# Kernel optimization log

Measured on AMD Instinct MI355X. Metric: run time of the kernel, lower is better.

Reference implementation:

```python
import jax, jax.numpy as jnp
import numpy as np

B, T, E, H, S = 64, 128, 256, 512, 1024


def setup_inputs() -> dict:
    key = jax.random.key(0)
    ks = jax.random.split(key, 14)
    p = lambda k, shape, s=0.05: jax.random.normal(k, shape, dtype=jnp.float32) * s
    return {
        "embedded_inputs": jax.random.normal(ks[0], (B, T, E), dtype=jnp.float32),
        "h0": jax.random.normal(ks[1], (B, H), dtype=jnp.float32),
        "c0": jax.random.normal(ks[2], (B, H), dtype=jnp.float32),
        "context": jax.random.normal(ks[3], (B, S, H), dtype=jnp.float32),
        "W_ih": p(ks[4], (E, 4 * H)),
        "b_ih": p(ks[5], (4 * H,)),
        "W_hh": p(ks[6], (H, 4 * H)),
        "b_hh": p(ks[7], (4 * H,)),
        "W_out": p(ks[8], (2 * H, H)),
        "b_out": p(ks[9], (H,)),
        "W_ax": p(ks[10], (H + E, H)),
        "b_ax": p(ks[11], (H,)),
        "W_pg": p(ks[12], (4 * H, 1)),
        "b_pg": p(ks[13], (1,)),
    }


def reference(embedded_inputs, h0, c0, context, W_ih, b_ih, W_hh, b_hh,
              W_out, b_out, W_ax, b_ax, W_pg, b_pg):
    # mask positions where the encoder output is all-zero padding
    ctx_mask = jnp.mean(context, axis=-1) == 0  # [B,S]

    def step(carry, x):  # x: [B,E]
        h, c = carry
        gates = x @ W_ih + b_ih + h @ W_hh + b_hh          # [B,4H]
        i, f, g, o = jnp.split(gates, 4, axis=-1)
        c_t = jax.nn.sigmoid(f) * c + jax.nn.sigmoid(i) * jnp.tanh(g)
        h_t = jax.nn.sigmoid(o) * jnp.tanh(c_t)            # [B,H]
        # dot attention
        scores = jnp.einsum('bsh,bh->bs', context, h_t)    # [B,S]
        scores = jnp.where(ctx_mask, -jnp.inf, scores)
        attn_dist = jax.nn.softmax(scores, axis=1)         # [B,S]
        attn_ctx = jnp.einsum('bsh,bs->bh', context, attn_dist)  # [B,H]
        xa = jnp.concatenate([attn_ctx, x], axis=-1) @ W_ax + b_ax   # [B,H]
        out = jnp.concatenate([attn_ctx, h_t], axis=-1) @ W_out + b_out  # [B,H]
        p_gen = jax.nn.sigmoid(
            jnp.concatenate([attn_ctx, h_t, c_t, xa], axis=-1) @ W_pg + b_pg)  # [B,1]
        return (h_t, c_t), (out, attn_dist, p_gen)

    xs = jnp.swapaxes(embedded_inputs, 0, 1)  # [T,B,E]
    (h, c), (outputs, attn_dists, p_gens) = jax.lax.scan(step, (h0, c0), xs)
    return outputs, h, c, attn_dists, p_gens
```

## Files before the change

kernel.cpp:

```cpp
#include <hip/hip_runtime.h>

#define T_ 128
#define B_ 64
#define E_ 256
#define H_ 512
#define S_ 1024
#define G_ 2048
#define NCH 6
#define NBLK 512
#define ABLK 128
#define BLK 256
#define NGRP 16
#define BH (B_*H_)
#define PSTR 520
#define PARTBUF (B_*NCH*PSTR)

#define U_ARR   256
#define U_TOTAL (U_ARR + NBLK*16)

#define F_V1   8704
#define F_VX   (F_V1 + 512)
#define F_S0   (F_VX + 256)
#define F_H3   (F_S0 + 64)
#define F_C3   (F_H3 + 3*BH)
#define F_SC2  (F_C3 + 3*BH)
#define F_PART (F_SC2 + 2*B_*S_)
#define F_CTX16 (F_PART + 2*PARTBUF)
#define WS_MIN_BYTES ((size_t)F_CTX16*4)
#define WS_BF16_BYTES ((size_t)F_CTX16*4 + (size_t)B_*S_*H_*2)

#define O_OUT 0
#define O_H   ((size_t)T_*B_*H_)
#define O_C   (O_H + BH)
#define O_AD  (O_C + BH)
#define O_PG  (O_AD + (size_t)T_*B_*S_)

#define S_ACT   0
#define S_PART  3088
#define S_GATE  4112
#define SB_RED  0
#define SB_ML   2080
#define SB_BIAS 2088
#define C_ACTX  5136
#define C_H2    5648
#define C_PRT   6160
#define C_TMP   6416
#define C_V1    6424
#define POOLSZ  7200

#define NEG_INF (-__builtin_inff())

__device__ __forceinline__ float sigm(float x){ return 1.f/(1.f+__expf(-x)); }
__device__ __forceinline__ float tanh_(float x){ return 1.f - 2.f/(1.f+__expf(2.f*x)); }
__device__ __forceinline__ float wred(float v){
#pragma unroll
  for (int m = 1; m < 64; m <<= 1) v += __shfl_xor(v, m, 64);
  return v;
}
__device__ __forceinline__ float ald(const float* p){
  return __hip_atomic_load(p, __ATOMIC_RELAXED, __HIP_MEMORY_SCOPE_AGENT);
}
__device__ __forceinline__ void ast(float* p, float v){
  __hip_atomic_store(p, v, __ATOMIC_RELAXED, __HIP_MEMORY_SCOPE_AGENT);
}
__device__ __forceinline__ void ast64(unsigned long long* p, unsigned long long v){
  __hip_atomic_store(p, v, __ATOMIC_RELAXED, __HIP_MEMORY_SCOPE_AGENT);
}
__device__ __forceinline__ unsigned short b16rne(float f){
  unsigned u = __float_as_uint(f);
  unsigned r = u + 0x7fffu + ((u >> 16) & 1u);
  return (unsigned short)(r >> 16);
}
__device__ __forceinline__ void unp(unsigned w, float& lo, float& hi){
  lo = __uint_as_float(w << 16);
  hi = __uint_as_float(w & 0xffff0000u);
}

__device__ __forceinline__ void gbar(unsigned* W, unsigned ep){
  __syncthreads();
  const int tid = threadIdx.x, bid = blockIdx.x;
  if (tid == 0) {
    asm volatile("s_waitcnt vmcnt(0)" ::: "memory");
    __hip_atomic_store(&W[U_ARR + bid*16], ep, __ATOMIC_RELAXED, __HIP_MEMORY_SCOPE_AGENT);
  }
  if (bid == 0) {
    const int i0 = tid*2, i1 = i0+1;
    while (__hip_atomic_load(&W[U_ARR + i0*16], __ATOMIC_RELAXED, __HIP_MEMORY_SCOPE_AGENT) < ep)
      __builtin_amdgcn_s_sleep(2);
    while (__hip_atomic_load(&W[U_ARR + i1*16], __ATOMIC_RELAXED, __HIP_MEMORY_SCOPE_AGENT) < ep)
      __builtin_amdgcn_s_sleep(2);
    __syncthreads();
    if (tid < NGRP)
      __hip_atomic_store(&W[tid*16], ep, __ATOMIC_RELAXED, __HIP_MEMORY_SCOPE_AGENT);
  }
  if (tid == 0) {
    while (__hip_atomic_load(&W[(bid>>5)*16], __ATOMIC_RELAXED, __HIP_MEMORY_SCOPE_AGENT) < ep)
      __builtin_amdgcn_s_sleep(4);
  }
  __syncthreads();
}

__device__ void do_A(int t, int bid, int tid,
                     const float* __restrict__ emb, const float* __restrict__ Wih,
                     const float* __restrict__ bih, const float* __restrict__ Whh,
                     const float* __restrict__ bhh, float* __restrict__ F,
                     float* __restrict__ pool)
{
  const int bg = bid >> 3, ug = bid & 7;
  {
    const int r = tid >> 6, i = tid & 63;
    const float* xr = emb + ((size_t)(bg*4 + r)*T_ + t)*E_ + i*4;
    *(float4*)(pool + S_ACT + r*772 + i*4) = *(const float4*)xr;
    const float* hsrc = F + F_H3 + ((t+2)%3)*BH + (size_t)(bg*4 + r)*H_ + i*8;
    float4 h0v, h1v;
    h0v.x=ald(hsrc+0); h0v.y=ald(hsrc+1); h0v.z=ald(hsrc+2); h0v.w=ald(hsrc+3);
    h1v.x=ald(hsrc+4); h1v.y=ald(hsrc+5); h1v.z=ald(hsrc+6); h1v.w=ald(hsrc+7);
    *(float4*)(pool + S_ACT + r*772 + 256 + i*8)     = h0v;
    *(float4*)(pool + S_ACT + r*772 + 256 + i*8 + 4) = h1v;
  }
  __syncthreads();
  const int ks = tid >> 7, bl = (tid >> 5) & 3, cq = tid & 31;
  const int cgi1 = cq, cgi2 = cq + 32;
  const int col1 = ((cgi1 >> 4) << 9) + ug*64 + ((cgi1 & 15) << 2);
  const int col2 = ((cgi2 >> 4) << 9) + ug*64 + ((cgi2 & 15) << 2);
  float4 A1, A2;
  if (ks == 0) {
    const float4 x1 = *(const float4*)(bih + col1), y1 = *(const float4*)(bhh + col1);
    const float4 x2 = *(const float4*)(bih + col2), y2 = *(const float4*)(bhh + col2);
    A1.x=x1.x+y1.x; A1.y=x1.y+y1.y; A1.z=x1.z+y1.z; A1.w=x1.w+y1.w;
    A2.x=x2.x+y2.x; A2.y=x2.y+y2.y; A2.z=x2.z+y2.z; A2.w=x2.w+y2.w;
  } else { A1.x=A1.y=A1.z=A1.w=0.f; A2.x=A2.y=A2.z=A2.w=0.f; }
  const float* ap = pool + S_ACT + bl*772;
  if (ks == 0) {
    const float* w1 = Wih + col1; const float* w2 = Wih + col2;
#pragma unroll 8
    for (int k = 0; k < 256; ++k) {
      float a = ap[k];
      float4 v1 = *(const float4*)(w1 + (size_t)k*G_);
      float4 v2 = *(const float4*)(w2 + (size_t)k*G_);
      A1.x=fmaf(a,v1.x,A1.x); A1.y=fmaf(a,v1.y,A1.y); A1.z=fmaf(a,v1.z,A1.z); A1.w=fmaf(a,v1.w,A1.w);
      A2.x=fmaf(a,v2.x,A2.x); A2.y=fmaf(a,v2.y,A2.y); A2.z=fmaf(a,v2.z,A2.z); A2.w=fmaf(a,v2.w,A2.w);
    }
    const float* u1 = Whh + col1; const float* u2 = Whh + col2;
    const float* ap2 = ap + 256;
#pragma unroll 8
    for (int k = 0; k < 128; ++k) {
      float a = ap2[k];
      float4 v1 = *(const float4*)(u1 + (size_t)k*G_);
      float4 v2 = *(const float4*)(u2 + (size_t)k*G_);
      A1.x=fmaf(a,v1.x,A1.x); A1.y=fmaf(a,v1.y,A1.y); A1.z=fmaf(a,v1.z,A1.z); A1.w=fmaf(a,v1.w,A1.w);
      A2.x=fmaf(a,v2.x,A2.x); A2.y=fmaf(a,v2.y,A2.y); A2.z=fmaf(a,v2.z,A2.z); A2.w=fmaf(a,v2.w,A2.w);
    }
  } else {
    const float* u1 = Whh + (size_t)128*G_ + col1; const float* u2 = Whh + (size_t)128*G_ + col2;
    const float* ap2 = ap + 384;
#pragma unroll 8
    for (int k = 0; k < 384; ++k) {
      float a = ap2[k];
      float4 v1 = *(const float4*)(u1 + (size_t)k*G_);
      float4 v2 = *(const float4*)(u2 + (size_t)k*G_);
      A1.x=fmaf(a,v1.x,A1.x); A1.y=fmaf(a,v1.y,A1.y); A1.z=fmaf(a,v1.z,A1.z); A1.w=fmaf(a,v1.w,A1.w);
      A2.x=fmaf(a,v2.x,A2.x); A2.y=fmaf(a,v2.y,A2.y); A2.z=fmaf(a,v2.z,A2.z); A2.w=fmaf(a,v2.w,A2.w);
    }
  }
  if (ks == 1) {
    *(float4*)(pool + S_PART + ((bl*64 + cgi1) << 2)) = A1;
    *(float4*)(pool + S_PART + ((bl*64 + cgi2) << 2)) = A2;
  }
  __syncthreads();
  if (ks == 0) {
    const float4 P1 = *(const float4*)(pool + S_PART + ((bl*64 + cgi1) << 2));
    const float4 P2 = *(const float4*)(pool + S_PART + ((bl*64 + cgi2) << 2));
    A1.x+=P1.x; A1.y+=P1.y; A1.z+=P1.z; A1.w+=P1.w;
    A2.x+=P2.x; A2.y+=P2.y; A2.z+=P2.z; A2.w+=P2.w;
    *(float4*)(pool + S_GATE + bl*256 + (cgi1 << 2)) = A1;
    *(float4*)(pool + S_GATE + bl*256 + (cgi2 << 2)) = A2;
  }
  __syncthreads();
  {
    const int bl2 = tid >> 6, ul = tid & 63;
    const int b2 = bg*4 + bl2, uu = ug*64 + ul;
    float gi = pool[S_GATE + bl2*256 + ul];
    float gf = pool[S_GATE + bl2*256 + 64 + ul];
    float gg = pool[S_GATE + bl2*256 + 128 + ul];
    float go = pool[S_GATE + bl2*256 + 192 + ul];
    float cp = ald(F + F_C3 + ((t+2)%3)*BH + (size_t)b2*H_ + uu);
    float cn = sigm(gf)*cp + sigm(gi)*tanh_(gg);
    float hn = sigm(go)*tanh_(cn);
    ast(F + F_H3 + (t%3)*BH + (size_t)b2*H_ + uu, hn);
    ast(F + F_C3 + (t%3)*BH + (size_t)b2*H_ + uu, cn);
  }
}

template<bool BF16>
__device__ void do_B(int t, int bid, int tid, const float* __restrict__ ctx,
                     float* __restrict__ F, float* __restrict__ pool)
{
  const int idx = bid - ABLK;
  const int b = idx / NCH, ch = idx - b*NCH;
  const int sb = (ch*S_)/NCH, se = ((ch+1)*S_)/NCH;
  const int w = tid >> 6, lane = tid & 63;
  const float* hb = F + F_H3 + (t%3)*BH + (size_t)b*H_ + lane*8;
  float h0_=ald(hb+0), h1_=ald(hb+1), h2_=ald(hb+2), h3_=ald(hb+3),
        h4_=ald(hb+4), h5_=ald(hb+5), h6_=ald(hb+6), h7_=ald(hb+7);
  float* scw = F + F_SC2 + (size_t)(t&1)*(B_*S_) + (size_t)b*S_;
  const float* s_bias = pool + SB_BIAS;

  if (BF16) {
    const uint4* c16v = (const uint4*)(F + F_CTX16) + (size_t)b*S_*64 + lane;
    float l = 0.f;
    float a0=0,a1=0,a2=0,a3=0,a4=0,a5=0,a6=0,a7=0;
    for (int s0 = sb + w*8; s0 < se; s0 += 32) {
      uint4 q[8];
#pragma unroll
      for (int i = 0; i < 8; ++i) {
        int s = s0 + i;
        int ss = (s < se) ? s : sb;
        q[i] = c16v[(size_t)ss*64];
      }
      float d[8];
#pragma unroll
      for (int i = 0; i < 8; ++i) {
        float c0,c1,c2,c3,c4,c5,c6,c7;
        unp(q[i].x,c0,c1); unp(q[i].y,c2,c3); unp(q[i].z,c4,c5); unp(q[i].w,c6,c7);
        d[i] = c0*h0_+c1*h1_+c2*h2_+c3*h3_+c4*h4_+c5*h5_+c6*h6_+c7*h7_;
      }
#pragma unroll
      for (int mm = 1; mm < 64; mm <<= 1) {
        d[0]+=__shfl_xor(d[0],mm,64); d[1]+=__shfl_xor(d[1],mm,64);
        d[2]+=__shfl_xor(d[2],mm,64); d[3]+=__shfl_xor(d[3],mm,64);
        d[4]+=__shfl_xor(d[4],mm,64); d[5]+=__shfl_xor(d[5],mm,64);
        d[6]+=__shfl_xor(d[6],mm,64); d[7]+=__shfl_xor(d[7],mm,64);
      }
      float wg[8];
#pragma unroll
      for (int i = 0; i < 8; ++i) {
        int s = s0 + i;
        bool v = (s < se);
        float bias = v ? s_bias[s - sb] : NEG_INF;
        float sc = d[i] + bias;
        if (lane == 0 && v) ast(scw + s, sc);
        wg[i] = (bias == 0.f) ? __expf(fminf(sc, 80.f)) : 0.f;
        l += wg[i];
      }
#pragma unroll
      for (int i = 0; i < 8; ++i) {
        float c0,c1,c2,c3,c4,c5,c6,c7;
        unp(q[i].x,c0,c1); unp(q[i].y,c2,c3); unp(q[i].z,c4,c5); unp(q[i].w,c6,c7);
        a0=fmaf(wg[i],c0,a0); a1=fmaf(wg[i],c1,a1); a2=fmaf(wg[i],c2,a2); a3=fmaf(wg[i],c3,a3);
        a4=fmaf(wg[i],c4,a4); a5=fmaf(wg[i],c5,a5); a6=fmaf(wg[i],c6,a6); a7=fmaf(wg[i],c7,a7);
      }
    }
    if (lane == 0) pool[SB_ML + w] = l;
    { float* r = pool + SB_RED + w*520 + lane*8;
      r[0]=a0; r[1]=a1; r[2]=a2; r[3]=a3; r[4]=a4; r[5]=a5; r[6]=a6; r[7]=a7; }
    __syncthreads();
    float lb = pool[SB_ML+0]+pool[SB_ML+1]+pool[SB_ML+2]+pool[SB_ML+3];
    float* Pp = F + F_PART + (size_t)(t&1)*PARTBUF + (size_t)(b*NCH+ch)*PSTR;
    for (int u = tid; u < H_; u += BLK)
      ast(Pp + 8 + u, pool[SB_RED + 0*520 + u] + pool[SB_RED + 1*520 + u]
                    + pool[SB_RED + 2*520 + u] + pool[SB_RED + 3*520 + u]);
    if (tid == 0) { ast(Pp+0, 0.f); ast(Pp+1, lb); }
    return;
  }

  const float* cbase = ctx + (size_t)b*S_*H_ + lane*8;
  float m = NEG_INF, l = 0.f;
  float a0=0,a1=0,a2=0,a3=0,a4=0,a5=0,a6=0,a7=0;
  for (int s0 = sb + w*4; s0 < se; s0 += 16) {
    float cv[4][8]; float d[4];
#pragma unroll
    for (int i = 0; i < 4; ++i) {
      int s = s0 + i;
      const float* cr = cbase + (size_t)(s < se ? s : sb)*H_;
      float4 cA = *(const float4*)cr, cB = *(const float4*)(cr + 4);
      cv[i][0]=cA.x; cv[i][1]=cA.y; cv[i][2]=cA.z; cv[i][3]=cA.w;
      cv[i][4]=cB.x; cv[i][5]=cB.y; cv[i][6]=cB.z; cv[i][7]=cB.w;
    }
#pragma unroll
    for (int i = 0; i < 4; ++i)
      d[i] = cv[i][0]*h0_ + cv[i][1]*h1_ + cv[i][2]*h2_ + cv[i][3]*h3_
           + cv[i][4]*h4_ + cv[i][5]*h5_ + cv[i][6]*h6_ + cv[i][7]*h7_;
#pragma unroll
    for (int mm = 1; mm < 64; mm <<= 1) {
      d[0] += __shfl_xor(d[0], mm, 64); d[1] += __shfl_xor(d[1], mm, 64);
      d[2] += __shfl_xor(d[2], mm, 64); d[3] += __shfl_xor(d[3], mm, 64);
    }
    float sc[4];
#pragma unroll
    for (int i = 0; i < 4; ++i) {
      int s = s0 + i;
      sc[i] = (s < se) ? d[i] + s_bias[s - sb] : NEG_INF;
      if (lane == 0 && s < se) ast(scw + s, sc[i]);
    }
    float mx = fmaxf(fmaxf(sc[0],sc[1]), fmaxf(sc[2],sc[3]));
    float mn = fmaxf(m, mx);
    float al = (mn == m) ? 1.f : __expf(m - mn);
    float w0 = (sc[0]==NEG_INF)?0.f:__expf(sc[0]-mn);
    float w1 = (sc[1]==NEG_INF)?0.f:__expf(sc[1]-mn);
    float w2 = (sc[2]==NEG_INF)?0.f:__expf(sc[2]-mn);
    float w3 = (sc[3]==NEG_INF)?0.f:__expf(sc[3]-mn);
    l = l*al + (w0+w1+w2+w3);
    a0 = a0*al + w0*cv[0][0] + w1*cv[1][0] + w2*cv[2][0] + w3*cv[3][0];
    a1 = a1*al + w0*cv[0][1] + w1*cv[1][1] + w2*cv[2][1] + w3*cv[3][1];
    a2 = a2*al + w0*cv[0][2] + w1*cv[1][2] + w2*cv[2][2] + w3*cv[3][2];
    a3 = a3*al + w0*cv[0][3] + w1*cv[1][3] + w2*cv[2][3] + w3*cv[3][3];
    a4 = a4*al + w0*cv[0][4] + w1*cv[1][4] + w2*cv[2][4] + w3*cv[3][4];
    a5 = a5*al + w0*cv[0][5] + w1*cv[1][5] + w2*cv[2][5] + w3*cv[3][5];
    a6 = a6*al + w0*cv[0][6] + w1*cv[1][6] + w2*cv[2][6] + w3*cv[3][6];
    a7 = a7*al + w0*cv[0][7] + w1*cv[1][7] + w2*cv[2][7] + w3*cv[3][7];
    m = mn;
  }
  if (lane == 0) { pool[SB_ML + w*2] = m; pool[SB_ML + w*2+1] = l; }
  { float* r = pool + SB_RED + w*520 + lane*8;
    r[0]=a0; r[1]=a1; r[2]=a2; r[3]=a3; r[4]=a4; r[5]=a5; r[6]=a6; r[7]=a7; }
  __syncthreads();
  float m0=pool[SB_ML+0], l0=pool[SB_ML+1], m1=pool[SB_ML+2], l1=pool[SB_ML+3],
        m2=pool[SB_ML+4], l2=pool[SB_ML+5], m3=pool[SB_ML+6], l3=pool[SB_ML+7];
  float mb = fmaxf(fmaxf(m0,m1), fmaxf(m2,m3));
  float k0 = (l0>0.f) ? __expf(m0-mb) : 0.f;
  float k1 = (l1>0.f) ? __expf(m1-mb) : 0.f;
  float k2 = (l2>0.f) ? __expf(m2-mb) : 0.f;
  float k3 = (l3>0.f) ? __expf(m3-mb) : 0.f;
  float lb = k0*l0 + k1*l1 + k2*l2 + k3*l3;
  float* Pp = F + F_PART + (size_t)(t&1)*PARTBUF + (size_t)(b*NCH+ch)*PSTR;
  for (int u = tid; u < H_; u += BLK)
    ast(Pp + 8 + u, k0*pool[SB_RED + 0*520 + u] + k1*pool[SB_RED + 1*520 + u]
                  + k2*pool[SB_RED + 2*520 + u] + k3*pool[SB_RED + 3*520 + u]);
  if (tid == 0) { ast(Pp+0, mb); ast(Pp+1, lb); }
}

__device__ void do_C(int tc, int bid, int tid,
                     const float* __restrict__ emb, const float* __restrict__ Wout,
                     const float* __restrict__ bout, const float* __restrict__ Wpg,
                     float* __restrict__ out, float* __restrict__ F,
                     float* __restrict__ pool)
{
  const int b = bid >> 1, p = bid & 1;
  const float* P0 = F + F_PART + (size_t)(tc&1)*PARTBUF + (size_t)(b*NCH)*PSTR;
  float mk[NCH], lk[NCH], ck[NCH];
  float mb = NEG_INF;
#pragma unroll
  for (int k = 0; k < NCH; ++k) { mk[k]=ald(P0+k*PSTR); lk[k]=ald(P0+k*PSTR+1); mb=fmaxf(mb,mk[k]); }
  float lb = 0.f;
#pragma unroll
  for (int k = 0; k < NCH; ++k) { ck[k] = (lk[k]>0.f) ? __expf(mk[k]-mb) : 0.f; lb += ck[k]*lk[k]; }
  float inv = 1.f/lb;
  {
    int u = tid;
    float v0 = 0.f, v1 = 0.f;
#pragma unroll
    for (int k = 0; k < NCH; ++k) {
      v0 += ck[k]*ald(P0 + k*PSTR + 8 + u);
      v1 += ck[k]*ald(P0 + k*PSTR + 8 + u + 256);
    }
    pool[C_ACTX + u]       = v0*inv;
    pool[C_ACTX + u + 256] = v1*inv;
    const float* hsrc = F + F_H3 + (tc%3)*BH + (size_t)b*H_;
    pool[C_H2 + tid]       = ald(hsrc + tid);
    pool[C_H2 + tid + 256] = ald(hsrc + tid + 256);
  }
  __syncthreads();
  {
    const float* scr = F + F_SC2 + (size_t)(tc&1)*(B_*S_) + (size_t)b*S_;
    float* ad = out + O_AD + ((size_t)tc*B_ + b)*S_;
    int s = p*512 + tid;
    ad[s] = __expf(ald(scr+s)-mb)*inv;
    s += 256;
    ad[s] = __expf(ald(scr+s)-mb)*inv;
  }
  {
    const int kh = tid >> 7, jj = tid & 127;
    const int j = p*256 + jj;
    float acc0 = (kh == 0) ? bout[j]     : 0.f;
    float acc1 = (kh == 0) ? bout[j+128] : 0.f;
    const float* src = (kh == 0) ? (pool + C_ACTX) : (pool + C_H2);
    const float* wq = Wout + (size_t)(kh*512)*H_ + j;
#pragma unroll 8
    for (int k = 0; k < 512; ++k) {
      float s = src[k];
      const float* r = wq + (size_t)k*H_;
      acc0 = fmaf(s, r[0],   acc0);
      acc1 = fmaf(s, r[128], acc1);
    }
    if (kh == 1) { pool[C_PRT + jj*2] = acc0; pool[C_PRT + jj*2 + 1] = acc1; }
    __syncthreads();
    if (kh == 0) {
      acc0 += pool[C_PRT + jj*2];
      acc1 += pool[C_PRT + jj*2 + 1];
      out[O_OUT + ((size_t)tc*B_ + b)*H_ + j]       = acc0;
      out[O_OUT + ((size_t)tc*B_ + b)*H_ + j + 128] = acc1;
    }
  }
  if (p == 0) {
    const float* cb = F + F_C3 + (tc%3)*BH + (size_t)b*H_;
    const float* xr = emb + ((size_t)b*T_ + tc)*E_;
    float part = 0.f;
#pragma unroll
    for (int jj2 = 0; jj2 < 7; ++jj2) {
      int i = tid + jj2*BLK;
      float v;
      if (i < 512)       v = pool[C_ACTX + i]     * pool[C_V1 + i];
      else if (i < 1024) v = pool[C_H2 + i - 512] * Wpg[i];
      else if (i < 1536) v = ald(cb + i - 1024)   * Wpg[i];
      else               v = xr[i - 1536]         * pool[C_V1 + 512 + (i - 1536)];
      part += v;
    }
    part = wred(part);
    if ((tid & 63) == 0) pool[C_TMP + (tid>>6)] = part;
    __syncthreads();
    if (tid == 0)
      out[O_PG + (size_t)tc*B_ + b] =
        sigm(pool[C_TMP]+pool[C_TMP+1]+pool[C_TMP+2]+pool[C_TMP+3] + pool[C_V1 + 768]);
  }
}

template<bool BF16>
__global__ __launch_bounds__(BLK, 2)
void decoder_kernel(const float* __restrict__ emb, const float* __restrict__ h0,
                    const float* __restrict__ c0, const float* __restrict__ ctx,
                    const float* __restrict__ Wih, const float* __restrict__ bih,
                    const float* __restrict__ Whh, const float* __restrict__ bhh,
                    const float* __restrict__ Wout, const float* __restrict__ bout,
                    const float* __restrict__ Wax, const float* __restrict__ bax,
                    const float* __restrict__ Wpg, const float* __restrict__ bpg,
                    float* __restrict__ out, float* __restrict__ F)
{
  __shared__ float pool[POOLSZ];
  unsigned* W = (unsigned*)F;
  const int tid = threadIdx.x, bid = blockIdx.x;
  unsigned ep = 0;

  if (bid < 128) {
    int i = bid*BLK + tid;
    ast(F + F_H3 + 2*BH + i, h0[i]);
    ast(F + F_C3 + 2*BH + i, c0[i]);
  }
  if (bid >= ABLK) {
    const int idx = bid - ABLK;
    const int b = idx / NCH, ch = idx - b*NCH;
    const int sb = (ch*S_)/NCH, se = ((ch+1)*S_)/NCH;
    const int w = tid >> 6, lane = tid & 63;
    for (int s = sb + w; s < se; s += 4) {
      const float* cr = ctx + ((size_t)b*S_ + s)*H_ + lane*8;
      float4 cA = *(const float4*)cr, cB = *(const float4*)(cr+4);
      float ssum = cA.x+cA.y+cA.z+cA.w+cB.x+cB.y+cB.z+cB.w;
      ssum = wred(ssum);
      if (lane == 0) pool[SB_BIAS + (s-sb)] = (ssum == 0.f) ? NEG_INF : 0.f;
    }
  }
  if (BF16) {
    unsigned long long* dst = (unsigned long long*)(F + F_CTX16);
    size_t base = (size_t)bid*BLK + tid;
#pragma unroll 2
    for (int it = 0; it < 32; ++it) {
      size_t ci = base + (size_t)it*131072;
      const float4 v0 = *(const float4*)(ctx + ci*8);
      const float4 v1 = *(const float4*)(ctx + ci*8 + 4);
      unsigned long long lo = (unsigned long long)b16rne(v0.x)
        | ((unsigned long long)b16rne(v0.y) << 16)
        | ((unsigned long long)b16rne(v0.z) << 32)
        | ((unsigned long long)b16rne(v0.w) << 48);
      unsigned long long hi = (unsigned long long)b16rne(v1.x)
        | ((unsigned long long)b16rne(v1.y) << 16)
        | ((unsigned long long)b16rne(v1.z) << 32)
        | ((unsigned long long)b16rne(v1.w) << 48);
      ast64(dst + ci*2, lo);
      ast64(dst + ci*2 + 1, hi);
    }
  }
  if (bid < 5) {
    const int w = tid>>6, lane = tid&63;
    const float* wp = Wpg + 1536 + lane*8;
    float4 wA = *(const float4*)wp, wB = *(const float4*)(wp+4);
    if (bid < 4) {
      for (int rr = 0; rr < 32; ++rr) {
        int k = bid*128 + rr*4 + w;
        const float* ar = Wax + (size_t)k*H_ + lane*8;
        float4 xA = *(const float4*)ar, xB = *(const float4*)(ar+4);
        float d = xA.x*wA.x+xA.y*wA.y+xA.z*wA.z+xA.w*wA.w
                + xB.x*wB.x+xB.y*wB.y+xB.z*wB.z+xB.w*wB.w;
        d = wred(d);
        if (lane == 0) ast(F + F_V1 + k, Wpg[k] + d);
      }
    } else {
      for (int rr = 0; rr < 64; ++rr) {
        int k = rr*4 + w;
        const float* ar = Wax + (size_t)(512+k)*H_ + lane*8;
        float4 xA = *(const float4*)ar, xB = *(const float4*)(ar+4);
        float d = xA.x*wA.x+xA.y*wA.y+xA.z*wA.z+xA.w*wA.w
                + xB.x*wB.x+xB.y*wB.y+xB.z*wB.z+xB.w*wB.w;
        d = wred(d);
        if (lane == 0) ast(F + F_VX + k, d);
      }
      if (tid < 64) {
        const float* br = bax + lane*8;
        float4 bA = *(const float4*)br, bB = *(const float4*)(br+4);
        float d = bA.x*wA.x+bA.y*wA.y+bA.z*wA.z+bA.w*wA.w
                + bB.x*wB.x+bB.y*wB.y+bB.z*wB.z+bB.w*wB.w;
        d = wred(d);
        if (lane == 0) ast(F + F_S0, bpg[0] + d);
      }
    }
  }
  gbar(W, ++ep);

  if (bid < ABLK) {
    for (int i = tid; i < 769; i += BLK)
      pool[C_V1 + i] = ald(F + F_V1 + i);
  }

  if (bid < ABLK) do_A(0, bid, tid, emb, Wih, bih, Whh, bhh, F, pool);
  gbar(W, ++ep);

  for (int t = 0; t < T_; ++t) {
    if (bid >= ABLK) {
      do_B<BF16>(t, bid, tid, ctx, F, pool);
    } else {
      if (t < T_-1) do_A(t+1, bid, tid, emb, Wih, bih, Whh, bhh, F, pool);
      if (t > 0)    do_C(t-1, bid, tid, emb, Wout, bout, Wpg, out, F, pool);
    }
    gbar(W, ++ep);
  }

  if (bid < ABLK) {
    do_C(T_-1, bid, tid, emb, Wout, bout, Wpg, out, F, pool);
  } else {
    const int idx = bid - ABLK;
    if (idx < 128) {
      int i = idx*BLK + tid;
      out[O_H + i] = ald(F + F_H3 + 1*BH + i);
    } else if (idx < 256) {
      int i = (idx-128)*BLK + tid;
      out[O_C + i] = ald(F + F_C3 + 1*BH + i);
    }
  }
}

extern "C" void kernel_launch(void* const* d_in, const int* in_sizes, int n_in,
                              void* d_out, int out_size, void* d_ws, size_t ws_size,
                              hipStream_t stream)
{
  if (ws_size < WS_MIN_BYTES) return;
  hipMemsetAsync(d_ws, 0, U_TOTAL * sizeof(unsigned), stream);
  if (ws_size >= WS_BF16_BYTES) {
    decoder_kernel<true><<<dim3(NBLK), dim3(BLK), 0, stream>>>(
        (const float*)d_in[0],  (const float*)d_in[1],  (const float*)d_in[2],
        (const float*)d_in[3],  (const float*)d_in[4],  (const float*)d_in[5],
        (const float*)d_in[6],  (const float*)d_in[7],  (const float*)d_in[8],
        (const float*)d_in[9],  (const float*)d_in[10], (const float*)d_in[11],
        (const float*)d_in[12], (const float*)d_in[13],
        (float*)d_out, (float*)d_ws);
  } else {
    decoder_kernel<false><<<dim3(NBLK), dim3(BLK), 0, stream>>>(
        (const float*)d_in[0],  (const float*)d_in[1],  (const float*)d_in[2],
        (const float*)d_in[3],  (const float*)d_in[4],  (const float*)d_in[5],
        (const float*)d_in[6],  (const float*)d_in[7],  (const float*)d_in[8],
        (const float*)d_in[9],  (const float*)d_in[10], (const float*)d_in[11],
        (const float*)d_in[12], (const float*)d_in[13],
        (float*)d_out, (float*)d_ws);
  }
}
```

Before: 7.485 ms.

## Double block size to 512 threads and re-split per-phase work across eight waves

Raises threads per block from 256 to 512 and reworks each phase to match. Attention blocks now stride over eight waves, and the output projection splits K four ways. The LSTM gate phase keeps only the first 256 threads active. The aim is more latency hiding and memory parallelism in the bandwidth-bound attention and output stages within the same persistent grid. In exchange, half the threads idle during the gate phase, barriers get larger, and register pressure rises under launch_bounds(512,4).

```diff
diff --git a/kernel.cpp b/kernel.cpp
--- a/kernel.cpp
+++ b/kernel.cpp
@@ -9,7 +9,7 @@
 #define NCH 6
 #define NBLK 512
 #define ABLK 128
-#define BLK 256
+#define BLK 512
 #define NGRP 16
 #define BH (B_*H_)
 #define PSTR 520
@@ -39,14 +39,14 @@
 #define S_PART  3088
 #define S_GATE  4112
 #define SB_RED  0
-#define SB_ML   2080
-#define SB_BIAS 2088
+#define SB_ML   4160
+#define SB_BIAS 4176
 #define C_ACTX  5136
 #define C_H2    5648
 #define C_PRT   6160
-#define C_TMP   6416
-#define C_V1    6424
-#define POOLSZ  7200
+#define C_TMP   6928
+#define C_V1    6936
+#define POOLSZ  7712
 
 #define NEG_INF (-__builtin_inff())
 
@@ -75,6 +75,11 @@
   lo = __uint_as_float(w << 16);
   hi = __uint_as_float(w & 0xffff0000u);
 }
+__device__ __forceinline__ unsigned long long pk8(const float4& v0, const float4& v1, int sel){
+  const float4& v = sel ? v1 : v0;
+  return (unsigned long long)b16rne(v.x) | ((unsigned long long)b16rne(v.y) << 16)
+       | ((unsigned long long)b16rne(v.z) << 32) | ((unsigned long long)b16rne(v.w) << 48);
+}
 
 __device__ __forceinline__ void gbar(unsigned* W, unsigned ep){
   __syncthreads();
@@ -84,11 +89,13 @@
     __hip_atomic_store(&W[U_ARR + bid*16], ep, __ATOMIC_RELAXED, __HIP_MEMORY_SCOPE_AGENT);
   }
   if (bid == 0) {
-    const int i0 = tid*2, i1 = i0+1;
-    while (__hip_atomic_load(&W[U_ARR + i0*16], __ATOMIC_RELAXED, __HIP_MEMORY_SCOPE_AGENT) < ep)
-      __builtin_amdgcn_s_sleep(2);
-    while (__hip_atomic_load(&W[U_ARR + i1*16], __ATOMIC_RELAXED, __HIP_MEMORY_SCOPE_AGENT) < ep)
-      __builtin_amdgcn_s_sleep(2);
+    if (tid < 256) {
+      const int i0 = tid*2, i1 = i0+1;
+      while (__hip_atomic_load(&W[U_ARR + i0*16], __ATOMIC_RELAXED, __HIP_MEMORY_SCOPE_AGENT) < ep)
+        __builtin_amdgcn_s_sleep(2);
+      while (__hip_atomic_load(&W[U_ARR + i1*16], __ATOMIC_RELAXED, __HIP_MEMORY_SCOPE_AGENT) < ep)
+        __builtin_amdgcn_s_sleep(2);
+    }
     __syncthreads();
     if (tid < NGRP)
       __hip_atomic_store(&W[tid*16], ep, __ATOMIC_RELAXED, __HIP_MEMORY_SCOPE_AGENT);
@@ -107,7 +114,7 @@
                      float* __restrict__ pool)
 {
   const int bg = bid >> 3, ug = bid & 7;
-  {
+  if (tid < 256) {
     const int r = tid >> 6, i = tid & 63;
     const float* xr = emb + ((size_t)(bg*4 + r)*T_ + t)*E_ + i*4;
     *(float4*)(pool + S_ACT + r*772 + i*4) = *(const float4*)xr;
@@ -119,56 +126,59 @@
     *(float4*)(pool + S_ACT + r*772 + 256 + i*8 + 4) = h1v;
   }
   __syncthreads();
-  const int ks = tid >> 7, bl = (tid >> 5) & 3, cq = tid & 31;
+  const int ks = (tid >> 7) & 1, bl = (tid >> 5) & 3, cq = tid & 31;
   const int cgi1 = cq, cgi2 = cq + 32;
   const int col1 = ((cgi1 >> 4) << 9) + ug*64 + ((cgi1 & 15) << 2);
   const int col2 = ((cgi2 >> 4) << 9) + ug*64 + ((cgi2 & 15) << 2);
   float4 A1, A2;
-  if (ks == 0) {
-    const float4 x1 = *(const float4*)(bih + col1), y1 = *(const float4*)(bhh + col1);
-    const float4 x2 = *(const float4*)(bih + col2), y2 = *(const float4*)(bhh + col2);
-    A1.x=x1.x+y1.x; A1.y=x1.y+y1.y; A1.z=x1.z+y1.z; A1.w=x1.w+y1.w;
-    A2.x=x2.x+y2.x; A2.y=x2.y+y2.y; A2.z=x2.z+y2.z; A2.w=x2.w+y2.w;
-  } else { A1.x=A1.y=A1.z=A1.w=0.f; A2.x=A2.y=A2.z=A2.w=0.f; }
-  const float* ap = pool + S_ACT + bl*772;
-  if (ks == 0) {
-    const float* w1 = Wih + col1; const float* w2 = Wih + col2;
+  A1.x=A1.y=A1.z=A1.w=0.f; A2.x=A2.y=A2.z=A2.w=0.f;
+  if (tid < 256) {
+    if (ks == 0) {
+      const float4 x1 = *(const float4*)(bih + col1), y1 = *(const float4*)(bhh + col1);
+      const float4 x2 = *(const float4*)(bih + col2), y2 = *(const float4*)(bhh + col2);
+      A1.x=x1.x+y1.x; A1.y=x1.y+y1.y; A1.z=x1.z+y1.z; A1.w=x1.w+y1.w;
+      A2.x=x2.x+y2.x; A2.y=x2.y+y2.y; A2.z=x2.z+y2.z; A2.w=x2.w+y2.w;
+    }
+    const float* ap = pool + S_ACT + bl*772;
+    if (ks == 0) {
+      const float* w1 = Wih + col1; const float* w2 = Wih + col2;
 #pragma unroll 8
-    for (int k = 0; k < 256; ++k) {
-      float a = ap[k];
-      float4 v1 = *(const float4*)(w1 + (size_t)k*G_);
-      float4 v2 = *(const float4*)(w2 + (size_t)k*G_);
-      A1.x=fmaf(a,v1.x,A1.x); A1.y=fmaf(a,v1.y,A1.y); A1.z=fmaf(a,v1.z,A1.z); A1.w=fmaf(a,v1.w,A1.w);
-      A2.x=fmaf(a,v2.x,A2.x); A2.y=fmaf(a,v2.y,A2.y); A2.z=fmaf(a,v2.z,A2.z); A2.w=fmaf(a,v2.w,A2.w);
-    }
-    const float* u1 = Whh + col1; const float* u2 = Whh + col2;
-    const float* ap2 = ap + 256;
+      for (int k = 0; k < 256; ++k) {
+        float a = ap[k];
+        float4 v1 = *(const float4*)(w1 + (size_t)k*G_);
+        float4 v2 = *(const float4*)(w2 + (size_t)k*G_);
+        A1.x=fmaf(a,v1.x,A1.x); A1.y=fmaf(a,v1.y,A1.y); A1.z=fmaf(a,v1.z,A1.z); A1.w=fmaf(a,v1.w,A1.w);
+        A2.x=fmaf(a,v2.x,A2.x); A2.y=fmaf(a,v2.y,A2.y); A2.z=fmaf(a,v2.z,A2.z); A2.w=fmaf(a,v2.w,A2.w);
+      }
+      const float* u1 = Whh + col1; const float* u2 = Whh + col2;
+      const float* ap2 = ap + 256;
 #pragma unroll 8
-    for (int k = 0; k < 128; ++k) {
-      float a = ap2[k];
-      float4 v1 = *(const float4*)(u1 + (size_t)k*G_);
-      float4 v2 = *(const float4*)(u2 + (size_t)k*G_);
-      A1.x=fmaf(a,v1.x,A1.x); A1.y=fmaf(a,v1.y,A1.y); A1.z=fmaf(a,v1.z,A1.z); A1.w=fmaf(a,v1.w,A1.w);
-      A2.x=fmaf(a,v2.x,A2.x); A2.y=fmaf(a,v2.y,A2.y); A2.z=fmaf(a,v2.z,A2.z); A2.w=fmaf(a,v2.w,A2.w);
-    }
-  } else {
-    const float* u1 = Whh + (size_t)128*G_ + col1; const float* u2 = Whh + (size_t)128*G_ + col2;
-    const float* ap2 = ap + 384;
+      for (int k = 0; k < 128; ++k) {
+        float a = ap2[k];
+        float4 v1 = *(const float4*)(u1 + (size_t)k*G_);
+        float4 v2 = *(const float4*)(u2 + (size_t)k*G_);
+        A1.x=fmaf(a,v1.x,A1.x); A1.y=fmaf(a,v1.y,A1.y); A1.z=fmaf(a,v1.z,A1.z); A1.w=fmaf(a,v1.w,A1.w);
+        A2.x=fmaf(a,v2.x,A2.x); A2.y=fmaf(a,v2.y,A2.y); A2.z=fmaf(a,v2.z,A2.z); A2.w=fmaf(a,v2.w,A2.w);
+      }
+    } else {
+      const float* u1 = Whh + (size_t)128*G_ + col1; const float* u2 = Whh + (size_t)128*G_ + col2;
+      const float* ap2 = ap + 384;
 #pragma unroll 8
-    for (int k = 0; k < 384; ++k) {
-      float a = ap2[k];
-      float4 v1 = *(const float4*)(u1 + (size_t)k*G_);
-      float4 v2 = *(const float4*)(u2 + (size_t)k*G_);
-      A1.x=fmaf(a,v1.x,A1.x); A1.y=fmaf(a,v1.y,A1.y); A1.z=fmaf(a,v1.z,A1.z); A1.w=fmaf(a,v1.w,A1.w);
-      A2.x=fmaf(a,v2.x,A2.x); A2.y=fmaf(a,v2.y,A2.y); A2.z=fmaf(a,v2.z,A2.z); A2.w=fmaf(a,v2.w,A2.w);
-    }
-  }
-  if (ks == 1) {
-    *(float4*)(pool + S_PART + ((bl*64 + cgi1) << 2)) = A1;
-    *(float4*)(pool + S_PART + ((bl*64 + cgi2) << 2)) = A2;
-  }
-  __syncthreads();
-  if (ks == 0) {
+      for (int k = 0; k < 384; ++k) {
+        float a = ap2[k];
+        float4 v1 = *(const float4*)(u1 + (size_t)k*G_);
+        float4 v2 = *(const float4*)(u2 + (size_t)k*G_);
+        A1.x=fmaf(a,v1.x,A1.x); A1.y=fmaf(a,v1.y,A1.y); A1.z=fmaf(a,v1.z,A1.z); A1.w=fmaf(a,v1.w,A1.w);
+        A2.x=fmaf(a,v2.x,A2.x); A2.y=fmaf(a,v2.y,A2.y); A2.z=fmaf(a,v2.z,A2.z); A2.w=fmaf(a,v2.w,A2.w);
+      }
+    }
+    if (ks == 1) {
+      *(float4*)(pool + S_PART + ((bl*64 + cgi1) << 2)) = A1;
+      *(float4*)(pool + S_PART + ((bl*64 + cgi2) << 2)) = A2;
+    }
+  }
+  __syncthreads();
+  if (tid < 256 && ks == 0) {
     const float4 P1 = *(const float4*)(pool + S_PART + ((bl*64 + cgi1) << 2));
     const float4 P2 = *(const float4*)(pool + S_PART + ((bl*64 + cgi2) << 2));
     A1.x+=P1.x; A1.y+=P1.y; A1.z+=P1.z; A1.w+=P1.w;
@@ -177,7 +187,7 @@
     *(float4*)(pool + S_GATE + bl*256 + (cgi2 << 2)) = A2;
   }
   __syncthreads();
-  {
+  if (tid < 256) {
     const int bl2 = tid >> 6, ul = tid & 63;
     const int b2 = bg*4 + bl2, uu = ug*64 + ul;
     float gi = pool[S_GATE + bl2*256 + ul];
@@ -210,7 +220,7 @@
     const uint4* c16v = (const uint4*)(F + F_CTX16) + (size_t)b*S_*64 + lane;
     float l = 0.f;
     float a0=0,a1=0,a2=0,a3=0,a4=0,a5=0,a6=0,a7=0;
-    for (int s0 = sb + w*8; s0 < se; s0 += 32) {
+    for (int s0 = sb + w*8; s0 < se; s0 += 64) {
       uint4 q[8];
 #pragma unroll
       for (int i = 0; i < 8; ++i) {
@@ -232,7 +242,6 @@
         d[4]+=__shfl_xor(d[4],mm,64); d[5]+=__shfl_xor(d[5],mm,64);
         d[6]+=__shfl_xor(d[6],mm,64); d[7]+=__shfl_xor(d[7],mm,64);
       }
-      float wg[8];
 #pragma unroll
       for (int i = 0; i < 8; ++i) {
         int s = s0 + i;
@@ -240,26 +249,30 @@
         float bias = v ? s_bias[s - sb] : NEG_INF;
         float sc = d[i] + bias;
         if (lane == 0 && v) ast(scw + s, sc);
-        wg[i] = (bias == 0.f) ? __expf(fminf(sc, 80.f)) : 0.f;
-        l += wg[i];
+        d[i] = (bias == 0.f) ? __expf(fminf(sc, 80.f)) : 0.f;
+        l += d[i];
       }
 #pragma unroll
       for (int i = 0; i < 8; ++i) {
         float c0,c1,c2,c3,c4,c5,c6,c7;
         unp(q[i].x,c0,c1); unp(q[i].y,c2,c3); unp(q[i].z,c4,c5); unp(q[i].w,c6,c7);
-        a0=fmaf(wg[i],c0,a0); a1=fmaf(wg[i],c1,a1); a2=fmaf(wg[i],c2,a2); a3=fmaf(wg[i],c3,a3);
-        a4=fmaf(wg[i],c4,a4); a5=fmaf(wg[i],c5,a5); a6=fmaf(wg[i],c6,a6); a7=fmaf(wg[i],c7,a7);
+        a0=fmaf(d[i],c0,a0); a1=fmaf(d[i],c1,a1); a2=fmaf(d[i],c2,a2); a3=fmaf(d[i],c3,a3);
+        a4=fmaf(d[i],c4,a4); a5=fmaf(d[i],c5,a5); a6=fmaf(d[i],c6,a6); a7=fmaf(d[i],c7,a7);
       }
     }
     if (lane == 0) pool[SB_ML + w] = l;
     { float* r = pool + SB_RED + w*520 + lane*8;
       r[0]=a0; r[1]=a1; r[2]=a2; r[3]=a3; r[4]=a4; r[5]=a5; r[6]=a6; r[7]=a7; }
     __syncthreads();
-    float lb = pool[SB_ML+0]+pool[SB_ML+1]+pool[SB_ML+2]+pool[SB_ML+3];
+    float lb = pool[SB_ML+0]+pool[SB_ML+1]+pool[SB_ML+2]+pool[SB_ML+3]
+             + pool[SB_ML+4]+pool[SB_ML+5]+pool[SB_ML+6]+pool[SB_ML+7];
     float* Pp = F + F_PART + (size_t)(t&1)*PARTBUF + (size_t)(b*NCH+ch)*PSTR;
-    for (int u = tid; u < H_; u += BLK)
-      ast(Pp + 8 + u, pool[SB_RED + 0*520 + u] + pool[SB_RED + 1*520 + u]
-                    + pool[SB_RED + 2*520 + u] + pool[SB_RED + 3*520 + u]);
+    for (int u = tid; u < H_; u += BLK) {
+      float s = 0.f;
+#pragma unroll
+      for (int w2 = 0; w2 < 8; ++w2) s += pool[SB_RED + w2*520 + u];
+      ast(Pp + 8 + u, s);
+    }
     if (tid == 0) { ast(Pp+0, 0.f); ast(Pp+1, lb); }
     return;
   }
@@ -267,7 +280,7 @@
   const float* cbase = ctx + (size_t)b*S_*H_ + lane*8;
   float m = NEG_INF, l = 0.f;
   float a0=0,a1=0,a2=0,a3=0,a4=0,a5=0,a6=0,a7=0;
-  for (int s0 = sb + w*4; s0 < se; s0 += 16) {
+  for (int s0 = sb + w*4; s0 < se; s0 += 32) {
     float cv[4][8]; float d[4];
 #pragma unroll
     for (int i = 0; i < 4; ++i) {
@@ -315,18 +328,23 @@
   { float* r = pool + SB_RED + w*520 + lane*8;
     r[0]=a0; r[1]=a1; r[2]=a2; r[3]=a3; r[4]=a4; r[5]=a5; r[6]=a6; r[7]=a7; }
   __syncthreads();
-  float m0=pool[SB_ML+0], l0=pool[SB_ML+1], m1=pool[SB_ML+2], l1=pool[SB_ML+3],
-        m2=pool[SB_ML+4], l2=pool[SB_ML+5], m3=pool[SB_ML+6], l3=pool[SB_ML+7];
-  float mb = fmaxf(fmaxf(m0,m1), fmaxf(m2,m3));
-  float k0 = (l0>0.f) ? __expf(m0-mb) : 0.f;
-  float k1 = (l1>0.f) ? __expf(m1-mb) : 0.f;
-  float k2 = (l2>0.f) ? __expf(m2-mb) : 0.f;
-  float k3 = (l3>0.f) ? __expf(m3-mb) : 0.f;
-  float lb = k0*l0 + k1*l1 + k2*l2 + k3*l3;
+  float mb = NEG_INF;
+#pragma unroll
+  for (int w2 = 0; w2 < 8; ++w2) mb = fmaxf(mb, pool[SB_ML + w2*2]);
+  float kk[8]; float lb = 0.f;
+#pragma unroll
+  for (int w2 = 0; w2 < 8; ++w2) {
+    float mw = pool[SB_ML + w2*2], lw = pool[SB_ML + w2*2 + 1];
+    kk[w2] = (lw > 0.f) ? __expf(mw - mb) : 0.f;
+    lb += kk[w2]*lw;
+  }
   float* Pp = F + F_PART + (size_t)(t&1)*PARTBUF + (size_t)(b*NCH+ch)*PSTR;
-  for (int u = tid; u < H_; u += BLK)
-    ast(Pp + 8 + u, k0*pool[SB_RED + 0*520 + u] + k1*pool[SB_RED + 1*520 + u]
-                  + k2*pool[SB_RED + 2*520 + u] + k3*pool[SB_RED + 3*520 + u]);
+  for (int u = tid; u < H_; u += BLK) {
+    float s = 0.f;
+#pragma unroll
+    for (int w2 = 0; w2 < 8; ++w2) s += kk[w2]*pool[SB_RED + w2*520 + u];
+    ast(Pp + 8 + u, s);
+  }
   if (tid == 0) { ast(Pp+0, mb); ast(Pp+1, lb); }
 }
 
@@ -348,46 +366,38 @@
   float inv = 1.f/lb;
   {
     int u = tid;
-    float v0 = 0.f, v1 = 0.f;
-#pragma unroll
-    for (int k = 0; k < NCH; ++k) {
-      v0 += ck[k]*ald(P0 + k*PSTR + 8 + u);
-      v1 += ck[k]*ald(P0 + k*PSTR + 8 + u + 256);
-    }
-    pool[C_ACTX + u]       = v0*inv;
-    pool[C_ACTX + u + 256] = v1*inv;
+    float v0 = 0.f;
+#pragma unroll
+    for (int k = 0; k < NCH; ++k) v0 += ck[k]*ald(P0 + k*PSTR + 8 + u);
+    pool[C_ACTX + u] = v0*inv;
     const float* hsrc = F + F_H3 + (tc%3)*BH + (size_t)b*H_;
-    pool[C_H2 + tid]       = ald(hsrc + tid);
-    pool[C_H2 + tid + 256] = ald(hsrc + tid + 256);
+    pool[C_H2 + u] = ald(hsrc + u);
   }
   __syncthreads();
   {
     const float* scr = F + F_SC2 + (size_t)(tc&1)*(B_*S_) + (size_t)b*S_;
-    float* ad = out + O_AD + ((size_t)tc*B_ + b)*S_;
     int s = p*512 + tid;
-    ad[s] = __expf(ald(scr+s)-mb)*inv;
-    s += 256;
-    ad[s] = __expf(ald(scr+s)-mb)*inv;
+    out[O_AD + ((size_t)tc*B_ + b)*S_ + s] = __expf(ald(scr+s)-mb)*inv;
   }
   {
-    const int kh = tid >> 7, jj = tid & 127;
+    const int q = tid >> 7, jj = tid & 127;
     const int j = p*256 + jj;
-    float acc0 = (kh == 0) ? bout[j]     : 0.f;
-    float acc1 = (kh == 0) ? bout[j+128] : 0.f;
-    const float* src = (kh == 0) ? (pool + C_ACTX) : (pool + C_H2);
-    const float* wq = Wout + (size_t)(kh*512)*H_ + j;
+    float acc0 = (q == 0) ? bout[j]     : 0.f;
+    float acc1 = (q == 0) ? bout[j+128] : 0.f;
+    const float* src = (q < 2) ? (pool + C_ACTX + q*256) : (pool + C_H2 + (q-2)*256);
+    const float* wq = Wout + (size_t)(q*256)*H_ + j;
 #pragma unroll 8
-    for (int k = 0; k < 512; ++k) {
+    for (int k = 0; k < 256; ++k) {
       float s = src[k];
       const float* r = wq + (size_t)k*H_;
       acc0 = fmaf(s, r[0],   acc0);
       acc1 = fmaf(s, r[128], acc1);
     }
-    if (kh == 1) { pool[C_PRT + jj*2] = acc0; pool[C_PRT + jj*2 + 1] = acc1; }
+    if (q > 0) { pool[C_PRT + (q-1)*256 + jj*2] = acc0; pool[C_PRT + (q-1)*256 + jj*2 + 1] = acc1; }
     __syncthreads();
-    if (kh == 0) {
-      acc0 += pool[C_PRT + jj*2];
-      acc1 += pool[C_PRT + jj*2 + 1];
+    if (q == 0) {
+      acc0 += pool[C_PRT + jj*2]       + pool[C_PRT + 256 + jj*2]       + pool[C_PRT + 512 + jj*2];
+      acc1 += pool[C_PRT + jj*2 + 1]   + pool[C_PRT + 256 + jj*2 + 1]   + pool[C_PRT + 512 + jj*2 + 1];
       out[O_OUT + ((size_t)tc*B_ + b)*H_ + j]       = acc0;
       out[O_OUT + ((size_t)tc*B_ + b)*H_ + j + 128] = acc1;
     }
@@ -397,26 +407,31 @@
     const float* xr = emb + ((size_t)b*T_ + tc)*E_;
     float part = 0.f;
 #pragma unroll
-    for (int jj2 = 0; jj2 < 7; ++jj2) {
+    for (int jj2 = 0; jj2 < 4; ++jj2) {
       int i = tid + jj2*BLK;
-      float v;
-      if (i < 512)       v = pool[C_ACTX + i]     * pool[C_V1 + i];
-      else if (i < 1024) v = pool[C_H2 + i - 512] * Wpg[i];
-      else if (i < 1536) v = ald(cb + i - 1024)   * Wpg[i];
-      else               v = xr[i - 1536]         * pool[C_V1 + 512 + (i - 1536)];
-      part += v;
+      if (i < 1792) {
+        float v;
+        if (i < 512)       v = pool[C_ACTX + i]     * pool[C_V1 + i];
+        else if (i < 1024) v = pool[C_H2 + i - 512] * Wpg[i];
+        else if (i < 1536) v = ald(cb + i - 1024)   * Wpg[i];
+        else               v = xr[i - 1536]         * pool[C_V1 + 512 + (i - 1536)];
+        part += v;
+      }
     }
     part = wred(part);
     if ((tid & 63) == 0) pool[C_TMP + (tid>>6)] = part;
     __syncthreads();
-    if (tid == 0)
-      out[O_PG + (size_t)tc*B_ + b] =
-        sigm(pool[C_TMP]+pool[C_TMP+1]+pool[C_TMP+2]+pool[C_TMP+3] + pool[C_V1 + 768]);
+    if (tid == 0) {
+      float s = pool[C_V1 + 768];
+#pragma unroll
+      for (int w2 = 0; w2 < 8; ++w2) s += pool[C_TMP + w2];
+      out[O_PG + (size_t)tc*B_ + b] = sigm(s);
+    }
   }
 }
 
 template<bool BF16>
-__global__ __launch_bounds__(BLK, 2)
+__global__ __launch_bounds__(BLK, 4)
 void decoder_kernel(const float* __restrict__ emb, const float* __restrict__ h0,
                     const float* __restrict__ c0, const float* __restrict__ ctx,
                     const float* __restrict__ Wih, const float* __restrict__ bih,
@@ -431,7 +446,7 @@
   const int tid = threadIdx.x, bid = blockIdx.x;
   unsigned ep = 0;
 
-  if (bid < 128) {
+  if (bid < 64) {
     int i = bid*BLK + tid;
     ast(F + F_H3 + 2*BH + i, h0[i]);
     ast(F + F_C3 + 2*BH + i, c0[i]);
@@ -441,7 +456,7 @@
     const int b = idx / NCH, ch = idx - b*NCH;
     const int sb = (ch*S_)/NCH, se = ((ch+1)*S_)/NCH;
     const int w = tid >> 6, lane = tid & 63;
-    for (int s = sb + w; s < se; s += 4) {
+    for (int s = sb + w; s < se; s += 8) {
       const float* cr = ctx + ((size_t)b*S_ + s)*H_ + lane*8;
       float4 cA = *(const float4*)cr, cB = *(const float4*)(cr+4);
       float ssum = cA.x+cA.y+cA.z+cA.w+cB.x+cB.y+cB.z+cB.w;
@@ -453,20 +468,12 @@
     unsigned long long* dst = (unsigned long long*)(F + F_CTX16);
     size_t base = (size_t)bid*BLK + tid;
 #pragma unroll 2
-    for (int it = 0; it < 32; ++it) {
-      size_t ci = base + (size_t)it*131072;
+    for (int it = 0; it < 16; ++it) {
+      size_t ci = base + (size_t)it*262144;
       const float4 v0 = *(const float4*)(ctx + ci*8);
       const float4 v1 = *(const float4*)(ctx + ci*8 + 4);
-      unsigned long long lo = (unsigned long long)b16rne(v0.x)
-        | ((unsigned long long)b16rne(v0.y) << 16)
-        | ((unsigned long long)b16rne(v0.z) << 32)
-        | ((unsigned long long)b16rne(v0.w) << 48);
-      unsigned long long hi = (unsigned long long)b16rne(v1.x)
-        | ((unsigned long long)b16rne(v1.y) << 16)
-        | ((unsigned long long)b16rne(v1.z) << 32)
-        | ((unsigned long long)b16rne(v1.w) << 48);
-      ast64(dst + ci*2, lo);
-      ast64(dst + ci*2 + 1, hi);
+      ast64(dst + ci*2,     pk8(v0, v1, 0));
+      ast64(dst + ci*2 + 1, pk8(v0, v1, 1));
     }
   }
   if (bid < 5) {
@@ -474,8 +481,8 @@
     const float* wp = Wpg + 1536 + lane*8;
     float4 wA = *(const float4*)wp, wB = *(const float4*)(wp+4);
     if (bid < 4) {
-      for (int rr = 0; rr < 32; ++rr) {
-        int k = bid*128 + rr*4 + w;
+      for (int rr = 0; rr < 16; ++rr) {
+        int k = bid*128 + rr*8 + w;
         const float* ar = Wax + (size_t)k*H_ + lane*8;
         float4 xA = *(const float4*)ar, xB = *(const float4*)(ar+4);
         float d = xA.x*wA.x+xA.y*wA.y+xA.z*wA.z+xA.w*wA.w
@@ -484,8 +491,8 @@
         if (lane == 0) ast(F + F_V1 + k, Wpg[k] + d);
       }
     } else {
-      for (int rr = 0; rr < 64; ++rr) {
-        int k = rr*4 + w;
+      for (int rr = 0; rr < 32; ++rr) {
+        int k = rr*8 + w;
         const float* ar = Wax + (size_t)(512+k)*H_ + lane*8;
         float4 xA = *(const float4*)ar, xB = *(const float4*)(ar+4);
         float d = xA.x*wA.x+xA.y*wA.y+xA.z*wA.z+xA.w*wA.w
@@ -527,11 +534,11 @@
     do_C(T_-1, bid, tid, emb, Wout, bout, Wpg, out, F, pool);
   } else {
     const int idx = bid - ABLK;
-    if (idx < 128) {
+    if (idx < 64) {
       int i = idx*BLK + tid;
       out[O_H + i] = ald(F + F_H3 + 1*BH + i);
-    } else if (idx < 256) {
-      int i = (idx-128)*BLK + tid;
+    } else if (idx < 128) {
+      int i = (idx-64)*BLK + tid;
       out[O_C + i] = ald(F + F_C3 + 1*BH + i);
     }
   }
@@ -543,21 +550,17 @@
 {
   if (ws_size < WS_MIN_BYTES) return;
   hipMemsetAsync(d_ws, 0, U_TOTAL * sizeof(unsigned), stream);
+#define ARGS \
+      (const float*)d_in[0],  (const float*)d_in[1],  (const float*)d_in[2],   \
+      (const float*)d_in[3],  (const float*)d_in[4],  (const float*)d_in[5],   \
+      (const float*)d_in[6],  (const float*)d_in[7],  (const float*)d_in[8],   \
+      (const float*)d_in[9],  (const float*)d_in[10], (const float*)d_in[11],  \
+      (const float*)d_in[12], (const float*)d_in[13],                          \
+      (float*)d_out, (float*)d_ws
   if (ws_size >= WS_BF16_BYTES) {
-    decoder_kernel<true><<<dim3(NBLK), dim3(BLK), 0, stream>>>(
-        (const float*)d_in[0],  (const float*)d_in[1],  (const float*)d_in[2],
-        (const float*)d_in[3],  (const float*)d_in[4],  (const float*)d_in[5],
-        (const float*)d_in[6],  (const float*)d_in[7],  (const float*)d_in[8],
-        (const float*)d_in[9],  (const float*)d_in[10], (const float*)d_in[11],
-        (const float*)d_in[12], (const float*)d_in[13],
-        (float*)d_out, (float*)d_ws);
+    decoder_kernel<true><<<dim3(NBLK), dim3(BLK), 0, stream>>>(ARGS);
   } else {
-    decoder_kernel<false><<<dim3(NBLK), dim3(BLK), 0, stream>>>(
-        (const float*)d_in[0],  (const float*)d_in[1],  (const float*)d_in[2],
-        (const float*)d_in[3],  (const float*)d_in[4],  (const float*)d_in[5],
-        (const float*)d_in[6],  (const float*)d_in[7],  (const float*)d_in[8],
-        (const float*)d_in[9],  (const float*)d_in[10], (const float*)d_in[11],
-        (const float*)d_in[12], (const float*)d_in[13],
-        (float*)d_out, (float*)d_ws);
-  }
-}
+    decoder_kernel<false><<<dim3(NBLK), dim3(BLK), 0, stream>>>(ARGS);
+  }
+#undef ARGS
+}
```

New measurement: 15.98 ms. 114% more time.
